# Optimization experiments

Hardware: AMD Instinct MI355X
Metric: run time of the kernel (lower is better)

The kernel has to match this reference:

```python
import jax, jax.numpy as jnp
import numpy as np

N, T, HW = 32, 46, 128
VOCAB_Q, NUM_ANS = 96, 32
WVEC, RNN_DIM = 32, 128
CNN_DIM, G_DIM, F_DIM = 24, 256, 256
G_IN = 2 * (CNN_DIM + 2) + RNN_DIM  # 180
BN_EPS = 1e-5


def setup_inputs() -> dict:
    key = jax.random.key(0)
    ks = jax.random.split(key, 16)
    s = 0.05
    rn = lambda k, shape: jax.random.normal(k, shape, dtype=jnp.float32) * s
    z = lambda shape: jnp.zeros(shape, jnp.float32)
    o = lambda shape: jnp.ones(shape, jnp.float32)
    inp = {}
    inp['questions'] = jax.random.randint(ks[0], (N, T), 1, VOCAB_Q)  # no NULL padding -> last step is the valid hidden state
    inp['images'] = jax.random.normal(ks[1], (N, 3, HW, HW), dtype=jnp.float32)
    inp['embed_W'] = rn(ks[2], (VOCAB_Q, WVEC))
    inp['lstm_Wih'] = rn(ks[3], (4 * RNN_DIM, WVEC))
    inp['lstm_Whh'] = rn(ks[4], (4 * RNN_DIM, RNN_DIM))
    inp['lstm_bih'] = z((4 * RNN_DIM,))
    inp['lstm_bhh'] = z((4 * RNN_DIM,))
    inp['conv0_W'] = rn(ks[5], (CNN_DIM, 3, 3, 3))
    inp['conv0_b'] = z((CNN_DIM,))
    inp['bn0_g'] = o((CNN_DIM,))
    inp['bn0_b'] = z((CNN_DIM,))
    inp['convs_W'] = rn(ks[6], (3, CNN_DIM, CNN_DIM, 3, 3))
    inp['convs_b'] = z((3, CNN_DIM))
    inp['bns_g'] = o((3, CNN_DIM))
    inp['bns_b'] = z((3, CNN_DIM))
    inp['g0_W'] = rn(ks[7], (G_DIM, G_IN))
    inp['g0_b'] = z((G_DIM,))
    inp['gs_W'] = rn(ks[8], (3, G_DIM, G_DIM))
    inp['gs_b'] = z((3, G_DIM))
    inp['f0_W'] = rn(ks[9], (F_DIM, G_DIM))
    inp['f0_b'] = z((F_DIM,))
    inp['f1_W'] = rn(ks[10], (F_DIM, F_DIM))
    inp['f1_b'] = z((F_DIM,))
    inp['f2_W'] = rn(ks[11], (NUM_ANS, F_DIM))
    inp['f2_b'] = z((NUM_ANS,))
    return inp


def _dense(x, W, b):
    return x @ W.T + b


def _lstm_last(emb, Wih, Whh, bih, bhh):
    # emb: (N, T, D); single-layer LSTM, PyTorch gate order (i, f, g, o); return last hidden state
    n, h = emb.shape[0], Whh.shape[1]
    bias = bih + bhh

    def step(carry, x_t):
        hp, cp = carry
        zg = x_t @ Wih.T + hp @ Whh.T + bias
        i, f, g, o_ = jnp.split(zg, 4, axis=-1)
        c = jax.nn.sigmoid(f) * cp + jax.nn.sigmoid(i) * jnp.tanh(g)
        hn = jax.nn.sigmoid(o_) * jnp.tanh(c)
        return (hn, c), None

    init = (jnp.zeros((n, h), emb.dtype), jnp.zeros((n, h), emb.dtype))
    (h_last, _), _ = jax.lax.scan(step, init, jnp.swapaxes(emb, 0, 1))
    return h_last


def _conv_bn_relu(x, W, b, gamma, beta):
    # Conv2d(k=3, s=2, p=1) + BatchNorm2d (training-mode batch stats) + ReLU
    x = jax.lax.conv_general_dilated(x, W, window_strides=(2, 2), padding=((1, 1), (1, 1)),
                                     dimension_numbers=('NCHW', 'OIHW', 'NCHW'))
    x = x + b[None, :, None, None]
    mu = x.mean((0, 2, 3), keepdims=True)
    var = ((x - mu) ** 2).mean((0, 2, 3), keepdims=True)  # biased var, as torch BN
    x = (x - mu) * jax.lax.rsqrt(var + BN_EPS)
    x = x * gamma[None, :, None, None] + beta[None, :, None, None]
    return jax.nn.relu(x)


def _forward(questions, images, embed_W, lstm_Wih, lstm_Whh, lstm_bih, lstm_bhh,
             conv0_W, conv0_b, bn0_g, bn0_b, convs_W, convs_b, bns_g, bns_b,
             g0_W, g0_b, gs_W, gs_b, f0_W, f0_b, f1_W, f1_b, f2_W, f2_b):
    # question encoder
    q_feats = _lstm_last(embed_W[questions], lstm_Wih, lstm_Whh, lstm_bih, lstm_bhh)  # (N, rnn_dim)
    # CNN stem
    x = _conv_bn_relu(images, conv0_W, conv0_b, bn0_g, bn0_b)
    for i in range(3):
        x = _conv_bn_relu(x, convs_W[i], convs_b[i], bns_g[i], bns_b[i])
    n, c, h, w = x.shape
    m = h * w
    # append normalized coordinates
    xc = jnp.broadcast_to(jnp.linspace(0.0, 1.0, w, dtype=x.dtype).reshape(1, 1, 1, w), (n, 1, h, w))
    yc = jnp.broadcast_to(jnp.linspace(0.0, 1.0, h, dtype=x.dtype).reshape(1, 1, h, 1), (n, 1, h, w))
    objects = jnp.concatenate([x, xc, yc], axis=1).reshape(n, c + 2, m)
    objects = jnp.swapaxes(objects, 1, 2)  # (N, M, C+2)
    # all M^2 ordered pairs: pairs[n, i*M+j] = [obj_i, obj_j]
    feats1 = jnp.repeat(objects, m, axis=1)        # (N, M^2, C+2)
    feats2 = jnp.tile(objects, (1, m, 1))          # (N, M^2, C+2)
    q_rep = jnp.broadcast_to(q_feats[:, None, :], (n, m * m, q_feats.shape[-1]))
    g_in = jnp.concatenate([feats1, feats2, q_rep], axis=-1)  # (N, M^2, 180)
    # shared MLP g
    hidden = jax.nn.relu(_dense(g_in, g0_W, g0_b))
    for i in range(3):
        hidden = jax.nn.relu(_dense(hidden, gs_W[i], gs_b[i]))
    f_in = hidden.sum(axis=1)  # old-torch sum(1) kept dim then [:,0] -> (N, g_dim)
    # MLP f (dropout = identity at eval)
    hidden = jax.nn.relu(_dense(f_in, f0_W, f0_b))
    hidden = jax.nn.relu(_dense(hidden, f1_W, f1_b))
    return _dense(hidden, f2_W, f2_b)  # (N, num_answers)


def reference(questions, images, embed_W, lstm_Wih, lstm_Whh, lstm_bih, lstm_bhh,
              conv0_W, conv0_b, bn0_g, bn0_b, convs_W, convs_b, bns_g, bns_b,
              g0_W, g0_b, gs_W, gs_b, f0_W, f0_b, f1_W, f1_b, f2_W, f2_b):
    return _forward(questions, images, embed_W, lstm_Wih, lstm_Whh, lstm_bih, lstm_bhh,
                    conv0_W, conv0_b, bn0_g, bn0_b, convs_W, convs_b, bns_g, bns_b,
                    g0_W, g0_b, gs_W, gs_b, f0_W, f0_b, f1_W, f1_b, f2_W, f2_b)
```

## Files before the change

kernel.cpp:

```cpp
#include <hip/hip_runtime.h>

#define NB   32
#define TT   46
#define RNN  128
#define CDIM 24
#define GD   256
#define GIN  180

typedef __attribute__((ext_vector_type(8))) short  bf16x8;
typedef __attribute__((ext_vector_type(4))) short  s16x4;
typedef __attribute__((ext_vector_type(8))) unsigned short u16x8;
typedef __attribute__((ext_vector_type(4))) float  f32x4;

__device__ __forceinline__ unsigned short f2bf(float v) {
    unsigned u = __float_as_uint(v);
    u = u + 0x7fffu + ((u >> 16) & 1u);
    return (unsigned short)(u >> 16);
}

__device__ __forceinline__ void lstm_body(
    const int* __restrict__ q, const float* __restrict__ embW,
    const float* __restrict__ Wih, const float* __restrict__ Whh,
    const float* __restrict__ bih, const float* __restrict__ bhh,
    float* __restrict__ qf, int n)
{
    const int tid = threadIdx.x;
    __shared__ float xs[32], hs[RNN], cs[RNN], zg[512];
    float wih[32], whh[RNN];
#pragma unroll
    for (int j = 0; j < 32; j++) wih[j] = Wih[tid * 32 + j];
#pragma unroll
    for (int j = 0; j < RNN; j++) whh[j] = Whh[tid * RNN + j];
    const float bias = bih[tid] + bhh[tid];
    if (tid < RNN) { hs[tid] = 0.f; cs[tid] = 0.f; }
    __syncthreads();
    for (int t = 0; t < TT; t++) {
        if (tid < 32) xs[tid] = embW[q[n * TT + t] * 32 + tid];
        __syncthreads();
        float acc = bias;
#pragma unroll
        for (int j = 0; j < 32; j++) acc += wih[j] * xs[j];
#pragma unroll
        for (int j = 0; j < RNN; j++) acc += whh[j] * hs[j];
        zg[tid] = acc;
        __syncthreads();
        if (tid < RNN) {
            float ig = 1.f / (1.f + expf(-zg[tid]));
            float fg = 1.f / (1.f + expf(-zg[RNN + tid]));
            float gg = tanhf(zg[2 * RNN + tid]);
            float og = 1.f / (1.f + expf(-zg[3 * RNN + tid]));
            float cn = fg * cs[tid] + ig * gg;
            cs[tid] = cn;
            hs[tid] = og * tanhf(cn);
        }
        __syncthreads();
    }
    if (tid < RNN) qf[n * RNN + tid] = hs[tid];
}

template<int CIN, int TILE, bool BNIN, int BS>
__device__ __forceinline__ void conv_body(
    const float* __restrict__ in, const float* __restrict__ Wg,
    const float* __restrict__ bias,
    const float* __restrict__ pstats, const float* __restrict__ pg,
    const float* __restrict__ pb, float pinvM,
    float* __restrict__ out, float* __restrict__ stats,
    int HIN, int WIN, int HO, int WO, int tilesX, int bx)
{
    constexpr int NPIX = TILE * TILE;
    constexpr int CPG  = BS / NPIX;
    constexpr int COPT = 24 / CPG;
    constexpr int WPB  = BS / 64;
    constexpr int WPC  = NPIX / 64;
    constexpr int S  = 2 * TILE + 1;
    constexpr int SP = S + 1;
    __shared__ float in_t[CIN][S][SP];
    __shared__ float r1s[WPB][COPT], r2s[WPB][COPT];
    __shared__ float sc[CIN], sh[CIN];
    const int tid = threadIdx.x;
    const int tx = bx % tilesX;
    const int ty = (bx / tilesX) % tilesX;
    const int n  = bx / (tilesX * tilesX);

    if (BNIN) {
        if (tid < CIN) {
            float mu  = pstats[2 * tid] * pinvM;
            float var = pstats[2 * tid + 1] * pinvM - mu * mu;
            float rs  = rsqrtf(var + 1e-5f);
            sc[tid] = rs * pg[tid];
            sh[tid] = pb[tid] - mu * rs * pg[tid];
        }
        __syncthreads();
    }
    const int iy0 = ty * 2 * TILE - 1, ix0 = tx * 2 * TILE - 1;
    for (int idx = tid; idx < CIN * S * S; idx += BS) {
        int ci = idx / (S * S), r = idx % (S * S);
        int ry = r / S, rx = r % S;
        int gy = iy0 + ry, gx = ix0 + rx;
        float v = 0.f;
        if ((unsigned)gy < (unsigned)HIN && (unsigned)gx < (unsigned)WIN) {
            v = in[((size_t)(n * CIN + ci) * HIN + gy) * WIN + gx];
            if (BNIN) v = fmaxf(v * sc[ci] + sh[ci], 0.f);
        }
        in_t[ci][ry][rx] = v;
    }
    __syncthreads();

    const int p   = tid % NPIX;
    const int co0 = __builtin_amdgcn_readfirstlane((tid / NPIX) * COPT);
    const int ly  = (p / TILE) * 2, lx = (p % TILE) * 2;
    float acc[COPT];
#pragma unroll
    for (int c = 0; c < COPT; c++) acc[c] = bias[co0 + c];
    for (int ci = 0; ci < CIN; ci++) {
#pragma unroll
        for (int ky = 0; ky < 3; ky++) {
            const float* row = &in_t[ci][ly + ky][lx];
#pragma unroll
            for (int kx = 0; kx < 3; kx++) {
                float v = row[kx];
#pragma unroll
                for (int c = 0; c < COPT; c++)
                    acc[c] += v * Wg[(((co0 + c) * CIN + ci) * 3 + ky) * 3 + kx];
            }
        }
    }
    const int oy = ty * TILE + p / TILE, ox = tx * TILE + p % TILE;
#pragma unroll
    for (int c = 0; c < COPT; c++)
        out[((size_t)(n * 24 + co0 + c) * HO + oy) * WO + ox] = acc[c];

    const int lane = tid & 63, wv = tid >> 6;
#pragma unroll
    for (int c = 0; c < COPT; c++) {
        float s1 = acc[c], s2 = acc[c] * acc[c];
#pragma unroll
        for (int off = 1; off < 64; off <<= 1) {
            s1 += __shfl_xor(s1, off, 64);
            s2 += __shfl_xor(s2, off, 64);
        }
        if (lane == 0) { r1s[wv][c] = s1; r2s[wv][c] = s2; }
    }
    __syncthreads();
    if (tid < 24) {
        int cg = tid / COPT, slot = tid % COPT;
        float t1 = 0.f, t2 = 0.f;
#pragma unroll
        for (int u = 0; u < WPC; u++) { t1 += r1s[cg * WPC + u][slot]; t2 += r2s[cg * WPC + u][slot]; }
        atomicAdd(&stats[tid * 2],     t1);
        atomicAdd(&stats[tid * 2 + 1], t2);
    }
}

template<int CIN, int TILE, bool BNIN>
__global__ __launch_bounds__(256) void conv_tiled(
    const float* __restrict__ in, const float* __restrict__ Wg,
    const float* __restrict__ bias,
    const float* __restrict__ pstats, const float* __restrict__ pg,
    const float* __restrict__ pb, float pinvM,
    float* __restrict__ out, float* __restrict__ stats,
    int HIN, int WIN, int HO, int WO, int tilesX)
{
    conv_body<CIN, TILE, BNIN, 256>(in, Wg, bias, pstats, pg, pb, pinvM,
                                    out, stats, HIN, WIN, HO, WO, tilesX, blockIdx.x);
}

__global__ __launch_bounds__(512) void fused_front(
    const int* __restrict__ q, const float* __restrict__ embW,
    const float* __restrict__ Wih, const float* __restrict__ Whh,
    const float* __restrict__ bih, const float* __restrict__ bhh,
    float* __restrict__ qf,
    const float* __restrict__ images, const float* __restrict__ c0W,
    const float* __restrict__ c0b, float* __restrict__ conv0o,
    float* __restrict__ stats,
    const float* __restrict__ gsW, unsigned short* __restrict__ Wbf)
{
    const int bx = blockIdx.x;
    if (bx < 32) {
        lstm_body(q, embW, Wih, Whh, bih, bhh, qf, bx);
    } else if (bx < 544) {
        conv_body<3, 16, false, 512>(images, c0W, c0b, nullptr, nullptr, nullptr, 0.f,
                                     conv0o, stats, 128, 128, 64, 64, 4, bx - 32);
    } else {
        int i = ((bx - 544) << 9) + threadIdx.x;
#pragma unroll
        for (int u = 0; u < 4; u++) {
            Wbf[i] = f2bf(gsW[i]);
            i += 96 * 512;
        }
    }
}

__global__ __launch_bounds__(256) void abqt_kernel(
    const float* __restrict__ feat,
    const float* __restrict__ stats, const float* __restrict__ g,
    const float* __restrict__ b, float invM,
    const float* __restrict__ qf,
    const float* __restrict__ g0W,
    const float* __restrict__ g0b,
    float* __restrict__ A, float* __restrict__ Bm, float* __restrict__ QT)
{
    const int n = blockIdx.x >> 2, iq = blockIdx.x & 3, k = threadIdx.x;
    __shared__ float obj[16][28];
    __shared__ float qs[RNN];
    __shared__ float sc[24], sh[24];
    if (k < 24) {
        float mu  = stats[2 * k] * invM;
        float var = stats[2 * k + 1] * invM - mu * mu;
        float rs  = rsqrtf(var + 1e-5f);
        sc[k] = rs * g[k];
        sh[k] = b[k] - mu * rs * g[k];
    }
    if (iq == 0 && k >= 128) qs[k - 128] = qf[n * RNN + (k - 128)];
    __syncthreads();
    for (int idx = k; idx < 24 * 16; idx += 256) {
        int c = idx >> 4, il = idx & 15;
        int i = (iq << 4) + il;
        float v = feat[(n * CDIM + c) * 64 + i];
        obj[il][c] = fmaxf(v * sc[c] + sh[c], 0.f);
    }
    if (k < 16) {
        int i = (iq << 4) + k;
        obj[k][24] = (float)(i & 7)  * (1.f / 7.f);
        obj[k][25] = (float)(i >> 3) * (1.f / 7.f);
        obj[k][26] = 0.f; obj[k][27] = 0.f;
    }
    __syncthreads();
    const float* wr = g0W + k * GIN;
    float wA[26], wB[26];
#pragma unroll
    for (int c = 0; c < 26; c++) { wA[c] = wr[c]; wB[c] = wr[26 + c]; }
    if (iq == 0) {
        float qv = g0b[k];
#pragma unroll
        for (int d = 0; d < RNN; d++) qv += wr[52 + d] * qs[d];
        QT[(n << 8) + k] = qv;
    }
    for (int il = 0; il < 16; il++) {
        const f32x4* op = (const f32x4*)obj[il];
        f32x4 r0 = op[0], r1 = op[1], r2 = op[2], r3 = op[3],
              r4 = op[4], r5 = op[5], r6 = op[6];
        float a = 0.f, bb = 0.f;
#pragma unroll
        for (int p = 0; p < 4; p++) {
            a += wA[p] * r0[p] + wA[4 + p] * r1[p] + wA[8 + p] * r2[p]
               + wA[12 + p] * r3[p] + wA[16 + p] * r4[p] + wA[20 + p] * r5[p];
            bb += wB[p] * r0[p] + wB[4 + p] * r1[p] + wB[8 + p] * r2[p]
                + wB[12 + p] * r3[p] + wB[16 + p] * r4[p] + wB[20 + p] * r5[p];
        }
        a += wA[24] * r6[0] + wA[25] * r6[1];
        bb += wB[24] * r6[0] + wB[25] * r6[1];
        int i = (iq << 4) + il;
        A [(((n << 6) + i) << 8) + k] = a;
        Bm[(((n << 6) + i) << 8) + k] = bb;
    }
}

__global__ __launch_bounds__(512, 4) void gs_fused(
    const float* __restrict__ A, const float* __restrict__ Bm, const float* __restrict__ QT,
    const unsigned short* __restrict__ Wb,
    const float* __restrict__ gsb,
    float* __restrict__ partial)
{
    __shared__ __align__(16) unsigned short Xs[128 * 256];
    __shared__ float AQ[2][256];
    __shared__ float biasv[3][256];
    const int bb = blockIdx.x, n = bb >> 5, ip = bb & 31, tid = threadIdx.x;
    const int lane = tid & 63, w = tid >> 6, l15 = lane & 15, lh = lane >> 4;
    const int rh = w >> 2, cq = w & 3;

    if (tid < 256) {
        float qt = QT[(n << 8) + tid];
        AQ[0][tid] = A[(((n << 6) + ip * 2)     << 8) + tid] + qt;
        AQ[1][tid] = A[(((n << 6) + ip * 2 + 1) << 8) + tid] + qt;
        biasv[0][tid] = gsb[tid];
        biasv[1][tid] = gsb[256 + tid];
        biasv[2][tid] = gsb[512 + tid];
    }
    __syncthreads();

#pragma unroll
    for (int it = 0; it < 8; it++) {
        int task = tid + (it << 9);
        int r = task >> 5, g = task & 31;
        int isub = r >> 6, j = r & 63;
        const f32x4* bp = (const f32x4*)(Bm + (((n << 6) + j) << 8) + (g << 3));
        f32x4 b0 = bp[0], b1 = bp[1];
        u16x8 pk;
        int c0 = g << 3;
#pragma unroll
        for (int p = 0; p < 4; p++) {
            pk[p]     = f2bf(fmaxf(b0[p] + AQ[isub][c0 + p], 0.f));
            pk[p + 4] = f2bf(fmaxf(b1[p] + AQ[isub][c0 + 4 + p], 0.f));
        }
        *(u16x8*)((char*)Xs + r * 512 + ((g ^ (r & 7)) << 4)) = pk;
    }

    f32x4 acc[4][4];
    const f32x4 zero4 = {0.f, 0.f, 0.f, 0.f};
    for (int layer = 0; layer < 3; layer++) {
#pragma unroll
        for (int tc = 0; tc < 4; tc++)
#pragma unroll
            for (int sl = 0; sl < 4; sl++) acc[tc][sl] = zero4;
        const unsigned short* wbase = Wb + (layer << 16)
                                    + (((cq << 6) + l15) << 8) + (lh << 3);
        __syncthreads();
#pragma unroll
        for (int kb = 0; kb < 8; kb++) {
            bf16x8 wa[4];
#pragma unroll
            for (int tc = 0; tc < 4; tc++)
                wa[tc] = *(const bf16x8*)(wbase + (tc << 12) + (kb << 5));
            bf16x8 xf[4];
#pragma unroll
            for (int sl = 0; sl < 4; sl++) {
                int ar = (rh << 6) + (sl << 4) + l15;
                int au = ((kb << 2) + lh) ^ (ar & 7);
                xf[sl] = *(const bf16x8*)((const char*)Xs + ar * 512 + (au << 4));
            }
#pragma unroll
            for (int tc = 0; tc < 4; tc++)
#pragma unroll
                for (int sl = 0; sl < 4; sl++)
                    acc[tc][sl] = __builtin_amdgcn_mfma_f32_16x16x32_bf16(
                        wa[tc], xf[sl], acc[tc][sl], 0, 0, 0);
        }
        if (layer < 2) {
            __syncthreads();
#pragma unroll
            for (int tc = 0; tc < 4; tc++) {
                int c0 = (cq << 6) + (tc << 4) + (lh << 2);
                float b0 = biasv[layer][c0],     b1 = biasv[layer][c0 + 1];
                float b2 = biasv[layer][c0 + 2], b3 = biasv[layer][c0 + 3];
#pragma unroll
                for (int sl = 0; sl < 4; sl++) {
                    int row = (rh << 6) + (sl << 4) + l15;
                    s16x4 pk;
                    pk[0] = (short)f2bf(fmaxf(acc[tc][sl][0] + b0, 0.f));
                    pk[1] = (short)f2bf(fmaxf(acc[tc][sl][1] + b1, 0.f));
                    pk[2] = (short)f2bf(fmaxf(acc[tc][sl][2] + b2, 0.f));
                    pk[3] = (short)f2bf(fmaxf(acc[tc][sl][3] + b3, 0.f));
                    *(s16x4*)((char*)Xs + row * 512 + (((c0 >> 3) ^ (row & 7)) << 4)
                              + ((c0 & 7) << 1)) = pk;
                }
            }
        } else {
#pragma unroll
            for (int tc = 0; tc < 4; tc++) {
                int c0 = (cq << 6) + (tc << 4) + (lh << 2);
                f32x4 cs;
#pragma unroll
                for (int p = 0; p < 4; p++) {
                    float bv = biasv[2][c0 + p];
                    float s = 0.f;
#pragma unroll
                    for (int sl = 0; sl < 4; sl++) s += fmaxf(acc[tc][sl][p] + bv, 0.f);
                    s += __shfl_xor(s, 1, 64);
                    s += __shfl_xor(s, 2, 64);
                    s += __shfl_xor(s, 4, 64);
                    s += __shfl_xor(s, 8, 64);
                    cs[p] = s;
                }
                if (l15 == 0)
                    *(f32x4*)(partial + (size_t)(bb * 2 + rh) * 256 + c0) = cs;
            }
        }
    }
}

__global__ __launch_bounds__(256) void f_mlp(
    const float* __restrict__ partial,
    const float* __restrict__ f0W, const float* __restrict__ f0b,
    const float* __restrict__ f1W, const float* __restrict__ f1b,
    const float* __restrict__ f2W, const float* __restrict__ f2b,
    float* __restrict__ out)
{
    const int n = blockIdx.x, k = threadIdx.x;
    __shared__ float fin[256], h1[256], h2[256];
    float s = 0.f;
    for (int b = 0; b < 64; b++) s += partial[(size_t)(n * 64 + b) * 256 + k];
    fin[k] = s;
    __syncthreads();
    const float* wr = f0W + k * 256;
    float a = f0b[k];
    for (int c = 0; c < 256; c++) a += wr[c] * fin[c];
    h1[k] = fmaxf(a, 0.f);
    __syncthreads();
    wr = f1W + k * 256;
    a = f1b[k];
    for (int c = 0; c < 256; c++) a += wr[c] * h1[c];
    h2[k] = fmaxf(a, 0.f);
    __syncthreads();
    if (k < 32) {
        wr = f2W + k * 256;
        a = f2b[k];
        for (int c = 0; c < 256; c++) a += wr[c] * h2[c];
        out[n * 32 + k] = a;
    }
}

extern "C" void kernel_launch(void* const* d_in, const int* in_sizes, int n_in,
                              void* d_out, int out_size, void* d_ws, size_t ws_size,
                              hipStream_t stream)
{
    const int*   questions = (const int*)  d_in[0];
    const float* images = (const float*)d_in[1];
    const float* embW   = (const float*)d_in[2];
    const float* Wih    = (const float*)d_in[3];
    const float* Whh    = (const float*)d_in[4];
    const float* bih    = (const float*)d_in[5];
    const float* bhh    = (const float*)d_in[6];
    const float* c0W    = (const float*)d_in[7];
    const float* c0b    = (const float*)d_in[8];
    const float* bn0g   = (const float*)d_in[9];
    const float* bn0b   = (const float*)d_in[10];
    const float* csW    = (const float*)d_in[11];
    const float* csb    = (const float*)d_in[12];
    const float* bnsg   = (const float*)d_in[13];
    const float* bnsb   = (const float*)d_in[14];
    const float* g0W    = (const float*)d_in[15];
    const float* g0b    = (const float*)d_in[16];
    const float* gsW    = (const float*)d_in[17];
    const float* gsb    = (const float*)d_in[18];
    const float* f0W    = (const float*)d_in[19];
    const float* f0b    = (const float*)d_in[20];
    const float* f1W    = (const float*)d_in[21];
    const float* f1b    = (const float*)d_in[22];
    const float* f2W    = (const float*)d_in[23];
    const float* f2b    = (const float*)d_in[24];

    float* ws  = (float*)d_ws;
    float* out = (float*)d_out;

    float* conv0o = ws;
    float* conv1o = ws + 3145728;
    float* conv2o = ws + 3932160;
    float* conv3o = ws + 4128768;
    float* stats  = ws + 4177920;
    float* qf     = ws + 4178112;
    unsigned short* Wbf = (unsigned short*)(ws + 4182208);
    float* Abuf   = ws;
    float* Bbuf   = ws + 524288;
    float* QTb    = ws + 1048576;
    float* part   = ws + 1155072;

    hipMemsetAsync(stats, 0, 192 * sizeof(float), stream);

    fused_front<<<640, 512, 0, stream>>>(questions, embW, Wih, Whh, bih, bhh, qf,
                                         images, c0W, c0b, conv0o, stats, gsW, Wbf);
    conv_tiled<24, 8, true><<<512, 256, 0, stream>>>(
        conv0o, csW, csb, stats, bn0g, bn0b, 1.f / 131072.f,
        conv1o, stats + 48, 64, 64, 32, 32, 4);
    conv_tiled<24, 8, true><<<128, 256, 0, stream>>>(
        conv1o, csW + 5184, csb + 24, stats + 48, bnsg, bnsb, 1.f / 32768.f,
        conv2o, stats + 96, 32, 32, 16, 16, 2);
    conv_tiled<24, 8, true><<<32, 256, 0, stream>>>(
        conv2o, csW + 10368, csb + 48, stats + 96, bnsg + 24, bnsb + 24, 1.f / 8192.f,
        conv3o, stats + 144, 16, 16, 8, 8, 1);

    abqt_kernel<<<128, 256, 0, stream>>>(conv3o, stats + 144, bnsg + 48, bnsb + 48,
                                         1.f / 2048.f, qf, g0W, g0b, Abuf, Bbuf, QTb);
    gs_fused<<<1024, 512, 0, stream>>>(Abuf, Bbuf, QTb, Wbf, gsb, part);
    f_mlp<<<32, 256, 0, stream>>>(part, f0W, f0b, f1W, f1b, f2W, f2b, out);
}
```

Baseline: 337.7 us.

## Restructure gs_fused waves, prefetch MFMA operands, stage g0 weights, warp-reduce f MLP

Result: slower. 356.7 us (+5.7%).

```diff
diff --git a/kernel.cpp b/kernel.cpp
--- a/kernel.cpp
+++ b/kernel.cpp
@@ -201,6 +201,8 @@
     float* __restrict__ A, float* __restrict__ Bm, float* __restrict__ QT)
 {
     const int n = blockIdx.x >> 2, iq = blockIdx.x & 3, k = threadIdx.x;
+    __shared__ float wAB[256][53];
+    __shared__ float wq[64][128];
     __shared__ float obj[16][28];
     __shared__ float qs[RNN];
     __shared__ float sc[24], sh[24];
@@ -211,7 +213,15 @@
         sc[k] = rs * g[k];
         sh[k] = b[k] - mu * rs * g[k];
     }
-    if (iq == 0 && k >= 128) qs[k - 128] = qf[n * RNN + (k - 128)];
+    if (k >= 128) qs[k - 128] = qf[n * RNN + (k - 128)];
+    for (int idx = k; idx < 256 * 52; idx += 256) {
+        int kr = idx / 52, c = idx % 52;
+        wAB[kr][c] = g0W[kr * GIN + c];
+    }
+    for (int idx = k; idx < 64 * 128; idx += 256) {
+        int r = idx >> 7, d = idx & 127;
+        wq[r][d] = g0W[(((iq << 6) + r)) * GIN + 52 + d];
+    }
     __syncthreads();
     for (int idx = k; idx < 24 * 16; idx += 256) {
         int c = idx >> 4, il = idx & 15;
@@ -226,16 +236,16 @@
         obj[k][26] = 0.f; obj[k][27] = 0.f;
     }
     __syncthreads();
-    const float* wr = g0W + k * GIN;
+    if (k < 64) {
+        int kr = (iq << 6) + k;
+        float qv = g0b[kr];
+#pragma unroll
+        for (int d = 0; d < RNN; d++) qv += wq[k][d] * qs[d];
+        QT[(n << 8) + kr] = qv;
+    }
     float wA[26], wB[26];
 #pragma unroll
-    for (int c = 0; c < 26; c++) { wA[c] = wr[c]; wB[c] = wr[26 + c]; }
-    if (iq == 0) {
-        float qv = g0b[k];
-#pragma unroll
-        for (int d = 0; d < RNN; d++) qv += wr[52 + d] * qs[d];
-        QT[(n << 8) + k] = qv;
-    }
+    for (int c = 0; c < 26; c++) { wA[c] = wAB[k][c]; wB[c] = wAB[k][26 + c]; }
     for (int il = 0; il < 16; il++) {
         const f32x4* op = (const f32x4*)obj[il];
         f32x4 r0 = op[0], r1 = op[1], r2 = op[2], r3 = op[3],
@@ -256,7 +266,7 @@
     }
 }
 
-__global__ __launch_bounds__(512, 4) void gs_fused(
+__global__ __launch_bounds__(256, 2) void gs_fused(
     const float* __restrict__ A, const float* __restrict__ Bm, const float* __restrict__ QT,
     const unsigned short* __restrict__ Wb,
     const float* __restrict__ gsb,
@@ -265,11 +275,12 @@
     __shared__ __align__(16) unsigned short Xs[128 * 256];
     __shared__ float AQ[2][256];
     __shared__ float biasv[3][256];
-    const int bb = blockIdx.x, n = bb >> 5, ip = bb & 31, tid = threadIdx.x;
+    const int raw = blockIdx.x;
+    const int bb = (raw & 7) * 128 + (raw >> 3);
+    const int n = bb >> 5, ip = bb & 31, tid = threadIdx.x;
     const int lane = tid & 63, w = tid >> 6, l15 = lane & 15, lh = lane >> 4;
-    const int rh = w >> 2, cq = w & 3;
-
-    if (tid < 256) {
+
+    {
         float qt = QT[(n << 8) + tid];
         AQ[0][tid] = A[(((n << 6) + ip * 2)     << 8) + tid] + qt;
         AQ[1][tid] = A[(((n << 6) + ip * 2 + 1) << 8) + tid] + qt;
@@ -280,8 +291,8 @@
     __syncthreads();
 
 #pragma unroll
-    for (int it = 0; it < 8; it++) {
-        int task = tid + (it << 9);
+    for (int it = 0; it < 16; it++) {
+        int task = tid + (it << 8);
         int r = task >> 5, g = task & 31;
         int isub = r >> 6, j = r & 63;
         const f32x4* bp = (const f32x4*)(Bm + (((n << 6) + j) << 8) + (g << 3));
@@ -296,46 +307,61 @@
         *(u16x8*)((char*)Xs + r * 512 + ((g ^ (r & 7)) << 4)) = pk;
     }
 
-    f32x4 acc[4][4];
+    f32x4 acc[4][8];
     const f32x4 zero4 = {0.f, 0.f, 0.f, 0.f};
+    bf16x8 wa[4], wn[4], xa[8], xn[8];
     for (int layer = 0; layer < 3; layer++) {
 #pragma unroll
         for (int tc = 0; tc < 4; tc++)
 #pragma unroll
-            for (int sl = 0; sl < 4; sl++) acc[tc][sl] = zero4;
+            for (int sl = 0; sl < 8; sl++) acc[tc][sl] = zero4;
         const unsigned short* wbase = Wb + (layer << 16)
-                                    + (((cq << 6) + l15) << 8) + (lh << 3);
+                                    + (((w << 6) + l15) << 8) + (lh << 3);
+#pragma unroll
+        for (int tc = 0; tc < 4; tc++) wa[tc] = *(const bf16x8*)(wbase + (tc << 12));
         __syncthreads();
 #pragma unroll
+        for (int sl = 0; sl < 8; sl++) {
+            int ar = (sl << 4) + l15;
+            int au = lh ^ (ar & 7);
+            xa[sl] = *(const bf16x8*)((const char*)Xs + ar * 512 + (au << 4));
+        }
+#pragma unroll
         for (int kb = 0; kb < 8; kb++) {
-            bf16x8 wa[4];
+            if (kb < 7) {
+#pragma unroll
+                for (int tc = 0; tc < 4; tc++)
+                    wn[tc] = *(const bf16x8*)(wbase + (tc << 12) + ((kb + 1) << 5));
+#pragma unroll
+                for (int sl = 0; sl < 8; sl++) {
+                    int ar = (sl << 4) + l15;
+                    int au = (((kb + 1) << 2) + lh) ^ (ar & 7);
+                    xn[sl] = *(const bf16x8*)((const char*)Xs + ar * 512 + (au << 4));
+                }
+            }
 #pragma unroll
             for (int tc = 0; tc < 4; tc++)
-                wa[tc] = *(const bf16x8*)(wbase + (tc << 12) + (kb << 5));
-            bf16x8 xf[4];
-#pragma unroll
-            for (int sl = 0; sl < 4; sl++) {
-                int ar = (rh << 6) + (sl << 4) + l15;
-                int au = ((kb << 2) + lh) ^ (ar & 7);
-                xf[sl] = *(const bf16x8*)((const char*)Xs + ar * 512 + (au << 4));
+#pragma unroll
+                for (int sl = 0; sl < 8; sl++)
+                    acc[tc][sl] = __builtin_amdgcn_mfma_f32_16x16x32_bf16(
+                        wa[tc], xa[sl], acc[tc][sl], 0, 0, 0);
+            if (kb < 7) {
+#pragma unroll
+                for (int tc = 0; tc < 4; tc++) wa[tc] = wn[tc];
+#pragma unroll
+                for (int sl = 0; sl < 8; sl++) xa[sl] = xn[sl];
             }
-#pragma unroll
-            for (int tc = 0; tc < 4; tc++)
-#pragma unroll
-                for (int sl = 0; sl < 4; sl++)
-                    acc[tc][sl] = __builtin_amdgcn_mfma_f32_16x16x32_bf16(
-                        wa[tc], xf[sl], acc[tc][sl], 0, 0, 0);
         }
         if (layer < 2) {
             __syncthreads();
 #pragma unroll
             for (int tc = 0; tc < 4; tc++) {
-                int c0 = (cq << 6) + (tc << 4) + (lh << 2);
+                int c0 = (w << 6) + (tc << 4) + (lh << 2);
                 float b0 = biasv[layer][c0],     b1 = biasv[layer][c0 + 1];
                 float b2 = biasv[layer][c0 + 2], b3 = biasv[layer][c0 + 3];
 #pragma unroll
-                for (int sl = 0; sl < 4; sl++) {
-                    int row = (rh << 6) + (sl << 4) + l15;
+                for (int sl = 0; sl < 8; sl++) {
+                    int row = (sl << 4) + l15;
                     s16x4 pk;
                     pk[0] = (short)f2bf(fmaxf(acc[tc][sl][0] + b0, 0.f));
                     pk[1] = (short)f2bf(fmaxf(acc[tc][sl][1] + b1, 0.f));
@@ -348,22 +374,21 @@
         } else {
 #pragma unroll
             for (int tc = 0; tc < 4; tc++) {
-                int c0 = (cq << 6) + (tc << 4) + (lh << 2);
+                int c0 = (w << 6) + (tc << 4) + (lh << 2);
                 f32x4 cs;
 #pragma unroll
                 for (int p = 0; p < 4; p++) {
                     float bv = biasv[2][c0 + p];
                     float s = 0.f;
 #pragma unroll
-                    for (int sl = 0; sl < 4; sl++) s += fmaxf(acc[tc][sl][p] + bv, 0.f);
+                    for (int sl = 0; sl < 8; sl++) s += fmaxf(acc[tc][sl][p] + bv, 0.f);
                     s += __shfl_xor(s, 1, 64);
                     s += __shfl_xor(s, 2, 64);
                     s += __shfl_xor(s, 4, 64);
                     s += __shfl_xor(s, 8, 64);
                     cs[p] = s;
                 }
-                if (l15 == 0)
-                    *(f32x4*)(partial + (size_t)(bb * 2 + rh) * 256 + c0) = cs;
+                if (l15 == 0) *(f32x4*)(partial + (size_t)bb * 256 + c0) = cs;
             }
         }
     }
@@ -377,26 +402,45 @@
     float* __restrict__ out)
 {
     const int n = blockIdx.x, k = threadIdx.x;
+    const int lane = k & 63, w = k >> 6;
     __shared__ float fin[256], h1[256], h2[256];
     float s = 0.f;
-    for (int b = 0; b < 64; b++) s += partial[(size_t)(n * 64 + b) * 256 + k];
+    for (int b = 0; b < 32; b++) s += partial[(size_t)(n * 32 + b) * 256 + k];
     fin[k] = s;
     __syncthreads();
-    const float* wr = f0W + k * 256;
-    float a = f0b[k];
-    for (int c = 0; c < 256; c++) a += wr[c] * fin[c];
-    h1[k] = fmaxf(a, 0.f);
-    __syncthreads();
-    wr = f1W + k * 256;
-    a = f1b[k];
-    for (int c = 0; c < 256; c++) a += wr[c] * h1[c];
-    h2[k] = fmaxf(a, 0.f);
-    __syncthreads();
-    if (k < 32) {
-        wr = f2W + k * 256;
-        a = f2b[k];
-        for (int c = 0; c < 256; c++) a += wr[c] * h2[c];
-        out[n * 32 + k] = a;
+    {
+        f32x4 xv = *(const f32x4*)(fin + (lane << 2));
+        for (int kk = 0; kk < 64; kk++) {
+            int krow = (w << 6) + kk;
+            f32x4 wv = *(const f32x4*)(f0W + (krow << 8) + (lane << 2));
+            float p = wv[0] * xv[0] + wv[1] * xv[1] + wv[2] * xv[2] + wv[3] * xv[3];
+#pragma unroll
+            for (int off = 1; off < 64; off <<= 1) p += __shfl_xor(p, off, 64);
+            if (lane == 0) h1[krow] = fmaxf(p + f0b[krow], 0.f);
+        }
+    }
+    __syncthreads();
+    {
+        f32x4 xv = *(const f32x4*)(h1 + (lane << 2));
+        for (int kk = 0; kk < 64; kk++) {
+            int krow = (w << 6) + kk;
+            f32x4 wv = *(const f32x4*)(f1W + (krow << 8) + (lane << 2));
+            float p = wv[0] * xv[0] + wv[1] * xv[1] + wv[2] * xv[2] + wv[3] * xv[3];
+#pragma unroll
+            for (int off = 1; off < 64; off <<= 1) p += __shfl_xor(p, off, 64);
+            if (lane == 0) h2[krow] = fmaxf(p + f1b[krow], 0.f);
+        }
+    }
+    __syncthreads();
+    if (w == 0) {
+        f32x4 xv = *(const f32x4*)(h2 + (lane << 2));
+        for (int kk = 0; kk < 32; kk++) {
+            f32x4 wv = *(const f32x4*)(f2W + (kk << 8) + (lane << 2));
+            float p = wv[0] * xv[0] + wv[1] * xv[1] + wv[2] * xv[2] + wv[3] * xv[3];
+#pragma unroll
+            for (int off = 1; off < 64; off <<= 1) p += __shfl_xor(p, off, 64);
+            if (lane == 0) out[(n << 5) + kk] = p + f2b[kk];
+        }
     }
 }
 
@@ -461,6 +505,6 @@
 
     abqt_kernel<<<128, 256, 0, stream>>>(conv3o, stats + 144, bnsg + 48, bnsb + 48,
                                          1.f / 2048.f, qf, g0W, g0b, Abuf, Bbuf, QTb);
-    gs_fused<<<1024, 512, 0, stream>>>(Abuf, Bbuf, QTb, Wbf, gsb, part);
+    gs_fused<<<1024, 256, 0, stream>>>(Abuf, Bbuf, QTb, Wbf, gsb, part);
     f_mlp<<<32, 256, 0, stream>>>(part, f0W, f0b, f1W, f1b, f2W, f2b, out);
 }
```
